# Optimization experiments

Hardware: AMD Instinct MI355X
Metric: run time of the kernel (lower is better)

Reference implementation:

```python
import jax, jax.numpy as jnp
import numpy as np

D_X, D_H, N_I = 1024, 64, 16  # model dim, per-head dim (d_q=d_k=d_v), heads
BSZ, SEQ = 2, 2048


def _linear(x, W, b):
    return x @ W.T + b


def setup_inputs() -> dict:
    key = jax.random.key(0)
    ks = jax.random.split(key, 16)
    s_in = 1.0 / np.sqrt(D_X)
    s_hd = 1.0 / np.sqrt(N_I * D_H)
    return {
        "query": jax.random.normal(ks[0], (BSZ, SEQ, D_X), jnp.float32),
        "key": jax.random.normal(ks[1], (BSZ, SEQ, D_X), jnp.float32),
        "value": jax.random.normal(ks[2], (BSZ, SEQ, D_X), jnp.float32),
        "Wq": jax.random.normal(ks[3], (N_I * D_H, D_X), jnp.float32) * s_in,
        "bq": jnp.zeros((N_I * D_H,), jnp.float32),
        "Wk": jax.random.normal(ks[4], (N_I * D_H, D_X), jnp.float32) * s_in,
        "bk": jnp.zeros((N_I * D_H,), jnp.float32),
        "Wv": jax.random.normal(ks[5], (N_I * D_H, D_X), jnp.float32) * s_in,
        "bv": jnp.zeros((N_I * D_H,), jnp.float32),
        "Wxv": jax.random.normal(ks[6], (N_I * D_H, D_X), jnp.float32) * s_in,
        "bxv": jnp.zeros((N_I * D_H,), jnp.float32),
        "Wxo": jax.random.normal(ks[7], (D_X, N_I * D_H), jnp.float32) * s_hd,
        "bxo": jnp.zeros((D_X,), jnp.float32),
        "Wmo": jax.random.normal(ks[8], (D_X, N_I * D_H), jnp.float32) * s_hd,
        "bmo": jnp.zeros((D_X,), jnp.float32),
    }


def reference(query, key, value, Wq, bq, Wk, bk, Wv, bv, Wxv, bxv, Wxo, bxo, Wmo, bmo):
    bsz, seq, _ = query.shape

    def heads(x):  # (b, s, n_I*d) -> (b, h, s, d)
        return x.reshape(bsz, seq, N_I, D_H).transpose(0, 2, 1, 3)

    Q = heads(_linear(query, Wq, bq))
    K = heads(_linear(key, Wk, bk))
    V = heads(_linear(value, Wv, bv))

    dot = jnp.einsum('bhid,bhjd->bhij', Q, K) / jnp.sqrt(jnp.float32(D_H))
    attention = jax.nn.softmax(dot, axis=-1)  # dropout p=0 (eval)

    # use_xv=True: replace K with xV = W_xv(key) for the k_bar aggregation
    xV = heads(_linear(key, Wxv, bxv))

    k_bar = jnp.einsum('bhjd,bhij->bhid', xV, attention)
    v_bar = jnp.einsum('bhjd,bhij->bhid', V, attention)

    def merge(x):  # (b, h, s, d) -> (b, s, h*d)
        return x.transpose(0, 2, 1, 3).reshape(bsz, seq, N_I * D_H)

    x = _linear(merge(k_bar), Wxo, bxo)
    m = _linear(merge(v_bar), Wmo, bmo)
    return (x, m)
```

## Files before the change

### kernel.cpp

```cpp
#include <hip/hip_runtime.h>
#include <math.h>

typedef __bf16 bf16;
typedef __bf16 bf16x2 __attribute__((ext_vector_type(2)));
typedef __bf16 bf16x4 __attribute__((ext_vector_type(4)));
typedef __bf16 bf16x8 __attribute__((ext_vector_type(8)));
typedef float f32x4 __attribute__((ext_vector_type(4)));

#define SEQ 2048
#define DH 64
#define DX 1024
#define NH 16
#define LP 72

static __device__ __forceinline__ f32x4 mfma16(bf16x8 a, bf16x8 b, f32x4 c) {
    return __builtin_amdgcn_mfma_f32_16x16x32_bf16(a, b, c, 0, 0, 0);
}
static __device__ __forceinline__ bf16x8 cvt8(const float* __restrict__ p) {
    f32x4 a = *(const f32x4*)p;
    f32x4 b = *(const f32x4*)(p + 4);
    bf16x8 r;
    #pragma unroll
    for (int j = 0; j < 4; ++j) { r[j] = (bf16)a[j]; r[4 + j] = (bf16)b[j]; }
    return r;
}

#define GL16(gp, lp) __builtin_amdgcn_global_load_lds( \
    (const __attribute__((address_space(1))) void*)(gp), \
    (__attribute__((address_space(3))) void*)(lp), 16, 0, 0)


__global__ __launch_bounds__(256) void cvt_all(
    const float* __restrict__ q, const float* __restrict__ k,
    const float* __restrict__ v,
    const float* __restrict__ w0, const float* __restrict__ w1,
    const float* __restrict__ w2, const float* __restrict__ w3,
    const float* __restrict__ w4, const float* __restrict__ w5,
    bf16* __restrict__ out)
{
    const size_t i = (size_t)blockIdx.x * 2048 + threadIdx.x * 8;
    const int seg = (int)(i >> 20);
    const float* s;
    size_t off;
    if (seg < 4)       { s = q; off = i; }
    else if (seg < 8)  { s = k; off = i - (4ull << 20); }
    else if (seg < 12) { s = v; off = i - (8ull << 20); }
    else {
        const float* ww[6] = {w0, w1, w2, w3, w4, w5};
        s = ww[seg - 12]; off = i - ((size_t)seg << 20);
    }
    *(bf16x8*)(out + i) = cvt8(s + off);
}

struct G4 {
    const bf16* X[4]; const bf16* W[4]; const float* B[4];
    bf16* Yb[4]; float* Yf[4]; int xmode[4]; int ymode[4];
};

template<int BM>
__global__ __launch_bounds__(512) void gemm256(G4 a)
{
    constexpr int MREP = BM / 32;
    __shared__ __align__(16) bf16 As[2][BM * 64];
    __shared__ __align__(16) bf16 Bs[2][256 * 64];

    const int z = blockIdx.z;
    const bf16* __restrict__ X = a.X[z];
    const bf16* __restrict__ W = a.W[z];
    const int xmode = a.xmode[z], ymode = a.ymode[z];

    const int tid  = threadIdx.x;
    const int wid  = tid >> 6;
    const int lane = tid & 63;
    const int l16  = lane & 15;
    const int quad = lane >> 4;
    const int wm   = wid >> 2;
    const int wn   = wid & 3;

    const int nx = gridDim.x;
    const int nt = nx * gridDim.y;
    int t = blockIdx.x + nx * blockIdx.y;
    t = (t & 7) * (nt >> 3) + (t >> 3);
    const int n0 = (t % nx) * 256;
    const int m0 = (t / nx) * BM;

    const int srow8 = lane >> 3;
    const int sch   = (lane & 7) ^ srow8;

    f32x4 acc[MREP][4];
    #pragma unroll
    for (int i = 0; i < MREP; ++i)
        #pragma unroll
        for (int j = 0; j < 4; ++j) acc[i][j] = (f32x4){0.f,0.f,0.f,0.f};

    auto stage = [&](int buf, int kb) {
        #pragma unroll
        for (int g = 0; g < BM / 64; ++g) {
            const int row = g * 64 + wid * 8 + srow8;
            const bf16* src;
            if (xmode == 0) {
                src = X + (size_t)(m0 + row) * DX + kb * 64 + sch * 8;
            } else {
                const int m = m0 + row;
                const int b = m >> 11, s = m & 2047;
                src = X + ((size_t)(b * NH + kb) * SEQ + s) * DH + sch * 8;
            }
            GL16(src, &As[buf][(g * 64 + wid * 8) * 64]);
        }
        #pragma unroll
        for (int g = 0; g < 4; ++g) {
            const int row = g * 64 + wid * 8 + srow8;
            const bf16* src = W + (size_t)(n0 + row) * DX + kb * 64 + sch * 8;
            GL16(src, &Bs[buf][(g * 64 + wid * 8) * 64]);
        }
    };

    stage(0, 0);
    __syncthreads();

    int cur = 0;
    for (int kb = 0; kb < DX / 64; ++kb) {
        if (kb + 1 < DX / 64) stage(cur ^ 1, kb + 1);
        #pragma unroll
        for (int ks = 0; ks < 2; ++ks) {
            bf16x8 af[MREP], bfr[4];
            const int cc = (ks * 4 + quad) ^ (l16 & 7);
            #pragma unroll
            for (int mf = 0; mf < MREP; ++mf)
                af[mf] = *(const bf16x8*)&As[cur][(wm * (BM/2) + mf * 16 + l16) * 64 + cc * 8];
            #pragma unroll
            for (int nf = 0; nf < 4; ++nf)
                bfr[nf] = *(const bf16x8*)&Bs[cur][(wn * 64 + nf * 16 + l16) * 64 + cc * 8];
            #pragma unroll
            for (int mf = 0; mf < MREP; ++mf)
                #pragma unroll
                for (int nf = 0; nf < 4; ++nf)
                    acc[mf][nf] = mfma16(af[mf], bfr[nf], acc[mf][nf]);
        }
        __syncthreads();
        cur ^= 1;
    }

    #pragma unroll
    for (int nf = 0; nf < 4; ++nf) {
        const int col = n0 + wn * 64 + nf * 16 + l16;
        const float bvv = a.B[z][col];
        #pragma unroll
        for (int mf = 0; mf < MREP; ++mf) {
            #pragma unroll
            for (int r = 0; r < 4; ++r) {
                const int row = m0 + wm * (BM/2) + mf * 16 + quad * 4 + r;
                const float vv = acc[mf][nf][r] + bvv;
                if (ymode == 0) {
                    const int b = row >> 11, s = row & 2047;
                    const int h = col >> 6, d = col & 63;
                    a.Yb[z][((size_t)(b * NH + h) * SEQ + s) * DH + d] = (bf16)vv;
                } else {
                    a.Yf[z][(size_t)row * DX + col] = vv;
                }
            }
        }
    }
}

__global__ __launch_bounds__(512) void attn_pair(
    bf16* __restrict__ Q, const bf16* __restrict__ K,
    const bf16* __restrict__ V, const bf16* __restrict__ xV,
    bf16* __restrict__ VB)
{
    __shared__ __align__(16) bf16 Ks[2][64 * 64];
    __shared__ __align__(16) bf16 Vt [64 * LP];
    __shared__ __align__(16) bf16 xVt[64 * LP];
    __shared__ __align__(16) bf16 Pl[4][32 * LP];

    const int tid  = threadIdx.x;
    const int wid  = tid >> 6;
    const int lane = tid & 63;
    const int l16  = lane & 15;
    const int quad = lane >> 4;
    const int pair = wid >> 1;
    const int half = wid & 1;
    const size_t hb = ((size_t)blockIdx.z * NH + blockIdx.y) * SEQ * DH;
    const int qp = blockIdx.x * 128 + pair * 32;
    const int q0 = qp + half * 16;

    bf16x8 qf[2];
    #pragma unroll
    for (int ks = 0; ks < 2; ++ks)
        qf[ks] = *(const bf16x8*)(Q + hb + (size_t)(q0 + l16) * DH + ks*32 + quad*8);

    bf16x8 one8;
    #pragma unroll
    for (int j = 0; j < 8; ++j) one8[j] = (bf16)1.0f;

    f32x4 ov[2][4];
    f32x4 rsa[2];
    #pragma unroll
    for (int mf = 0; mf < 2; ++mf) {
        rsa[mf] = (f32x4){0.f,0.f,0.f,0.f};
        #pragma unroll
        for (int c = 0; c < 4; ++c) ov[mf][c] = (f32x4){0.f,0.f,0.f,0.f};
    }

    const int krow = lane >> 3;
    const int kch  = (lane & 7) ^ krow;
    const bf16* __restrict__ vsrc = (tid & 256) ? xV : V;
    bf16* __restrict__ vdst = (tid & 256) ? xVt : Vt;
    const int t8  = tid & 255;
    const int vkp = (t8 & 31) * 2;
    const int vd0 = (t8 >> 5) * 8;
    const float SCL = 0.125f * 1.4426950408889634f;

    bf16x8 pv0, pv1;
    {
        const bf16* kg = K + hb + (size_t)(wid*8 + krow) * DH + kch*8;
        GL16(kg, &Ks[0][(wid*8) * 64]);
        const size_t g0 = hb + (size_t)vkp * DH + vd0;
        pv0 = *(const bf16x8*)(vsrc + g0);
        pv1 = *(const bf16x8*)(vsrc + g0 + DH);
    }

    int c = 0;
    for (int kt = 0; kt < SEQ; kt += 64) {
        #pragma unroll
        for (int j = 0; j < 8; ++j)
            *(bf16x2*)&vdst[(vd0 + j) * LP + vkp] = (bf16x2){pv0[j], pv1[j]};
        if (kt + 64 < SEQ) {
            const bf16* kg = K + hb + (size_t)(kt + 64 + wid*8 + krow) * DH + kch*8;
            GL16(kg, &Ks[c ^ 1][(wid*8) * 64]);
            const size_t g0 = hb + (size_t)(kt + 64 + vkp) * DH + vd0;
            pv0 = *(const bf16x8*)(vsrc + g0);
            pv1 = *(const bf16x8*)(vsrc + g0 + DH);
        }
        __asm__ volatile("s_waitcnt lgkmcnt(0)" ::: "memory");
        __builtin_amdgcn_s_barrier();
        __asm__ volatile("s_waitcnt vmcnt(3)" ::: "memory");
        __builtin_amdgcn_sched_barrier(0);

        f32x4 sf[4];
        #pragma unroll
        for (int mf = 0; mf < 4; ++mf) sf[mf] = (f32x4){0.f,0.f,0.f,0.f};
        __builtin_amdgcn_s_setprio(1);
        #pragma unroll
        for (int ks = 0; ks < 2; ++ks)
            #pragma unroll
            for (int mf = 0; mf < 4; ++mf) {
                bf16x8 kf = *(const bf16x8*)&Ks[c][(mf*16 + l16) * 64 +
                                                   (((ks*4 + quad) ^ (l16 & 7)) * 8)];
                sf[mf] = mfma16(kf, qf[ks], sf[mf]);
            }
        __builtin_amdgcn_s_setprio(0);

        #pragma unroll
        for (int mf = 0; mf < 4; ++mf) {
            float p0 = __builtin_amdgcn_exp2f(sf[mf][0] * SCL);
            float p1 = __builtin_amdgcn_exp2f(sf[mf][1] * SCL);
            float p2 = __builtin_amdgcn_exp2f(sf[mf][2] * SCL);
            float p3 = __builtin_amdgcn_exp2f(sf[mf][3] * SCL);
            *(bf16x4*)&Pl[pair][(half*16 + l16) * LP + mf*16 + quad*4] =
                (bf16x4){(bf16)p0, (bf16)p1, (bf16)p2, (bf16)p3};
        }
        __asm__ volatile("s_waitcnt lgkmcnt(0)" ::: "memory");
        __builtin_amdgcn_s_barrier();
        __builtin_amdgcn_sched_barrier(0);

        __builtin_amdgcn_s_setprio(1);
        #pragma unroll
        for (int ks = 0; ks < 2; ++ks) {
            bf16x8 pa[2];
            #pragma unroll
            for (int mf = 0; mf < 2; ++mf)
                pa[mf] = *(const bf16x8*)&Pl[pair][(mf*16 + l16) * LP + ks*32 + quad*8];
            #pragma unroll
            for (int mf = 0; mf < 2; ++mf)
                rsa[mf] = mfma16(pa[mf], one8, rsa[mf]);
            const bf16* __restrict__ tile = half ? xVt : Vt;
            #pragma unroll
            for (int cc = 0; cc < 4; ++cc) {
                bf16x8 bv = *(const bf16x8*)&tile[(cc*16 + l16) * LP + ks*32 + quad*8];
                #pragma unroll
                for (int mf = 0; mf < 2; ++mf)
                    ov[mf][cc] = mfma16(pa[mf], bv, ov[mf][cc]);
            }
        }
        __builtin_amdgcn_s_setprio(0);

        __builtin_amdgcn_sched_barrier(0);
        __builtin_amdgcn_s_barrier();
        c ^= 1;
    }

    bf16* __restrict__ outp = half ? Q : VB;
    #pragma unroll
    for (int mf = 0; mf < 2; ++mf)
        #pragma unroll
        for (int r = 0; r < 4; ++r) {
            const int qrow = mf * 16 + quad * 4 + r;
            const float inv = 1.0f / rsa[mf][r];
            const size_t base = hb + (size_t)(qp + qrow) * DH;
            #pragma unroll
            for (int cc = 0; cc < 4; ++cc)
                outp[base + cc*16 + l16] = (bf16)(ov[mf][cc][r] * inv);
        }
}


__global__ __launch_bounds__(256) void proj_gemm(
    const void* __restrict__ Xv, const float* __restrict__ W,
    const float* __restrict__ bias, void* __restrict__ Yv,
    int in_kind, int out_mode)
{
    __shared__ __align__(16) bf16 As[64 * LP];
    __shared__ __align__(16) bf16 Bs[128 * LP];
    const int tid  = threadIdx.x;
    const int wave = tid >> 6;
    const int lane = tid & 63;
    const int l16  = lane & 15;
    const int quad = lane >> 4;
    const int m0 = blockIdx.y * 64;
    const int n0 = blockIdx.x * 128;
    const int m_w = (wave >> 1) * 32;
    const int n_w = (wave & 1) * 64;
    const int ar = tid >> 2, ac = (tid & 3) * 16;
    const int br = tid >> 1, bc = (tid & 1) * 32;

    f32x4 acc[2][4];
    #pragma unroll
    for (int i = 0; i < 2; ++i)
        #pragma unroll
        for (int j = 0; j < 4; ++j) acc[i][j] = (f32x4){0.f,0.f,0.f,0.f};

    for (int kb = 0; kb < DX / 64; ++kb) {
        __syncthreads();
        if (in_kind == 0) {
            const float* xp = (const float*)Xv + (size_t)(m0 + ar) * DX + kb * 64 + ac;
            *(bf16x8*)&As[ar * LP + ac]     = cvt8(xp);
            *(bf16x8*)&As[ar * LP + ac + 8] = cvt8(xp + 8);
        } else {
            const bf16* xp = (const bf16*)Xv + ((size_t)kb * SEQ + (m0 + ar)) * DH + ac;
            *(bf16x8*)&As[ar * LP + ac]     = *(const bf16x8*)xp;
            *(bf16x8*)&As[ar * LP + ac + 8] = *(const bf16x8*)(xp + 8);
        }
        {
            const float* wp = W + (size_t)(n0 + br) * DX + kb * 64 + bc;
            #pragma unroll
            for (int g = 0; g < 4; ++g)
                *(bf16x8*)&Bs[br * LP + bc + g * 8] = cvt8(wp + g * 8);
        }
        __syncthreads();
        #pragma unroll
        for (int ks = 0; ks < 2; ++ks) {
            bf16x8 a0 = *(const bf16x8*)&As[(m_w + l16)      * LP + ks * 32 + quad * 8];
            bf16x8 a1 = *(const bf16x8*)&As[(m_w + 16 + l16) * LP + ks * 32 + quad * 8];
            #pragma unroll
            for (int nf = 0; nf < 4; ++nf) {
                bf16x8 b = *(const bf16x8*)&Bs[(n_w + nf * 16 + l16) * LP + ks * 32 + quad * 8];
                acc[0][nf] = mfma16(a0, b, acc[0][nf]);
                acc[1][nf] = mfma16(a1, b, acc[1][nf]);
            }
        }
    }
    #pragma unroll
    for (int mf = 0; mf < 2; ++mf)
        #pragma unroll
        for (int nf = 0; nf < 4; ++nf) {
            const int col = n0 + n_w + nf * 16 + l16;
            const float bvv = bias[col];
            #pragma unroll
            for (int r = 0; r < 4; ++r) {
                const int row = m0 + m_w + mf * 16 + quad * 4 + r;
                float v = acc[mf][nf][r] + bvv;
                if (out_mode == 0) {
                    int h = col >> 6, d = col & 63;
                    ((bf16*)Yv)[((size_t)h * SEQ + row) * DH + d] = (bf16)v;
                } else {
                    ((float*)Yv)[(size_t)row * DX + col] = v;
                }
            }
        }
}

__global__ __launch_bounds__(256) void attn_dual(
    bf16* __restrict__ Q, const bf16* __restrict__ K,
    const bf16* __restrict__ V, const bf16* __restrict__ xV,
    bf16* __restrict__ vb)
{
    __shared__ __align__(16) bf16 Ks [64 * LP];
    __shared__ __align__(16) bf16 Vt [64 * LP];
    __shared__ __align__(16) bf16 xVt[64 * LP];
    __shared__ __align__(16) bf16 Pl[4][32 * LP];
    const int tid  = threadIdx.x;
    const int h    = blockIdx.y;
    const int qt   = blockIdx.x;
    const int wave = tid >> 6;
    const int lane = tid & 63;
    const int l16  = lane & 15;
    const int quad = lane >> 4;
    const size_t hb = (size_t)h * SEQ * DH;
    const int q0 = qt * 128 + wave * 32;

    bf16x8 qf[2][2];
    #pragma unroll
    for (int mf = 0; mf < 2; ++mf)
        #pragma unroll
        for (int ks = 0; ks < 2; ++ks)
            qf[mf][ks] = *(const bf16x8*)(Q + hb + (size_t)(q0 + mf*16 + l16) * DH + ks*32 + quad*8);

    float mr[2][4], lr[2][4];
    f32x4 ov[2][4], oxv[2][4];
    #pragma unroll
    for (int mf = 0; mf < 2; ++mf)
        #pragma unroll
        for (int r = 0; r < 4; ++r) { mr[mf][r] = -1e30f; lr[mf][r] = 0.f; }
    #pragma unroll
    for (int mf = 0; mf < 2; ++mf)
        #pragma unroll
        for (int c = 0; c < 4; ++c) {
            ov[mf][c]  = (f32x4){0.f,0.f,0.f,0.f};
            oxv[mf][c] = (f32x4){0.f,0.f,0.f,0.f};
        }
    const int sr = tid >> 2, sc = (tid & 3) * 16;
    const int vkp = (tid & 31) * 2;
    const int vd0 = (tid >> 5) * 8;
    const float SCL = 0.125f * 1.4426950408889634f;

    for (int kt = 0; kt < SEQ; kt += 64) {
        __syncthreads();
        {
            const bf16* kpt = K + hb + (size_t)(kt + sr) * DH + sc;
            *(bf16x8*)&Ks[sr * LP + sc]     = *(const bf16x8*)kpt;
            *(bf16x8*)&Ks[sr * LP + sc + 8] = *(const bf16x8*)(kpt + 8);
            const size_t g0 = hb + (size_t)(kt + vkp) * DH + vd0;
            bf16x8 v0 = *(const bf16x8*)(V + g0);
            bf16x8 v1 = *(const bf16x8*)(V + g0 + DH);
            bf16x8 x0 = *(const bf16x8*)(xV + g0);
            bf16x8 x1 = *(const bf16x8*)(xV + g0 + DH);
            #pragma unroll
            for (int j = 0; j < 8; ++j) {
                *(bf16x2*)&Vt [(vd0 + j) * LP + vkp] = (bf16x2){v0[j], v1[j]};
                *(bf16x2*)&xVt[(vd0 + j) * LP + vkp] = (bf16x2){x0[j], x1[j]};
            }
        }
        __syncthreads();
        f32x4 sf[2][4];
        #pragma unroll
        for (int mf = 0; mf < 2; ++mf)
            #pragma unroll
            for (int nf = 0; nf < 4; ++nf) sf[mf][nf] = (f32x4){0.f,0.f,0.f,0.f};
        #pragma unroll
        for (int ks = 0; ks < 2; ++ks)
            #pragma unroll
            for (int nf = 0; nf < 4; ++nf) {
                bf16x8 bk = *(const bf16x8*)&Ks[(nf * 16 + l16) * LP + ks * 32 + quad * 8];
                sf[0][nf] = mfma16(qf[0][ks], bk, sf[0][nf]);
                sf[1][nf] = mfma16(qf[1][ks], bk, sf[1][nf]);
            }
        float mx[2][4], rs[2][4], alpha[2][4];
        #pragma unroll
        for (int mf = 0; mf < 2; ++mf)
            #pragma unroll
            for (int r = 0; r < 4; ++r) {
                float aa = fmaxf(sf[mf][0][r], sf[mf][1][r]);
                float bb = fmaxf(sf[mf][2][r], sf[mf][3][r]);
                mx[mf][r] = fmaxf(aa, bb) * SCL;
            }
        #pragma unroll
        for (int off = 1; off < 16; off <<= 1)
            #pragma unroll
            for (int mf = 0; mf < 2; ++mf)
                #pragma unroll
                for (int r = 0; r < 4; ++r)
                    mx[mf][r] = fmaxf(mx[mf][r], __shfl_xor(mx[mf][r], off, 64));
        #pragma unroll
        for (int mf = 0; mf < 2; ++mf)
            #pragma unroll
            for (int r = 0; r < 4; ++r) {
                float mnew = fmaxf(mr[mf][r], mx[mf][r]);
                alpha[mf][r] = exp2f(mr[mf][r] - mnew);
                mr[mf][r] = mnew;
            }
        bf16* pw = &Pl[wave][0];
        #pragma unroll
        for (int mf = 0; mf < 2; ++mf)
            #pragma unroll
            for (int r = 0; r < 4; ++r) rs[mf][r] = 0.f;
        #pragma unroll
        for (int mf = 0; mf < 2; ++mf)
            #pragma unroll
            for (int nf = 0; nf < 4; ++nf)
                #pragma unroll
                for (int r = 0; r < 4; ++r) {
                    float p = exp2f(sf[mf][nf][r] * SCL - mr[mf][r]);
                    rs[mf][r] += p;
                    pw[(mf * 16 + quad * 4 + r) * LP + nf * 16 + l16] = (bf16)p;
                }
        #pragma unroll
        for (int off = 1; off < 16; off <<= 1)
            #pragma unroll
            for (int mf = 0; mf < 2; ++mf)
                #pragma unroll
                for (int r = 0; r < 4; ++r)
                    rs[mf][r] += __shfl_xor(rs[mf][r], off, 64);
        #pragma unroll
        for (int mf = 0; mf < 2; ++mf)
            #pragma unroll
            for (int r = 0; r < 4; ++r)
                lr[mf][r] = lr[mf][r] * alpha[mf][r] + rs[mf][r];
        #pragma unroll
        for (int mf = 0; mf < 2; ++mf)
            #pragma unroll
            for (int c = 0; c < 4; ++c)
                #pragma unroll
                for (int r = 0; r < 4; ++r) {
                    ov[mf][c][r]  *= alpha[mf][r];
                    oxv[mf][c][r] *= alpha[mf][r];
                }
        __asm__ volatile("s_waitcnt lgkmcnt(0)" ::: "memory");
        #pragma unroll
        for (int ks = 0; ks < 2; ++ks) {
            bf16x8 pa0 = *(const bf16x8*)&Pl[wave][(l16)      * LP + ks * 32 + quad * 8];
            bf16x8 pa1 = *(const bf16x8*)&Pl[wave][(16 + l16) * LP + ks * 32 + quad * 8];
            #pragma unroll
            for (int c = 0; c < 4; ++c) {
                bf16x8 bv = *(const bf16x8*)&Vt [(c * 16 + l16) * LP + ks * 32 + quad * 8];
                ov[0][c]  = mfma16(pa0, bv, ov[0][c]);
                ov[1][c]  = mfma16(pa1, bv, ov[1][c]);
                bf16x8 bx = *(const bf16x8*)&xVt[(c * 16 + l16) * LP + ks * 32 + quad * 8];
                oxv[0][c] = mfma16(pa0, bx, oxv[0][c]);
                oxv[1][c] = mfma16(pa1, bx, oxv[1][c]);
            }
        }
    }
    #pragma unroll
    for (int mf = 0; mf < 2; ++mf)
        #pragma unroll
        for (int r = 0; r < 4; ++r) {
            const int s = q0 + mf * 16 + quad * 4 + r;
            const float inv = 1.0f / lr[mf][r];
            #pragma unroll
            for (int c = 0; c < 4; ++c) {
                const int d = c * 16 + l16;
                Q [hb + (size_t)s * DH + d] = (bf16)(oxv[mf][c][r] * inv);
                vb[hb + (size_t)s * DH + d] = (bf16)(ov[mf][c][r]  * inv);
            }
        }
}


extern "C" void kernel_launch(void* const* d_in, const int* in_sizes, int n_in,
                              void* d_out, int out_size, void* d_ws, size_t ws_size,
                              hipStream_t stream) {
    const float* query = (const float*)d_in[0];
    const float* key   = (const float*)d_in[1];
    const float* value = (const float*)d_in[2];
    const float* Wq  = (const float*)d_in[3];  const float* bq  = (const float*)d_in[4];
    const float* Wk  = (const float*)d_in[5];  const float* bk  = (const float*)d_in[6];
    const float* Wv  = (const float*)d_in[7];  const float* bv  = (const float*)d_in[8];
    const float* Wxv = (const float*)d_in[9];  const float* bxv = (const float*)d_in[10];
    const float* Wxo = (const float*)d_in[11]; const float* bxo = (const float*)d_in[12];
    const float* Wmo = (const float*)d_in[13]; const float* bmo = (const float*)d_in[14];

    float* out = (float*)d_out;
    const size_t SB = (size_t)SEQ * DX;
    const size_t M1 = 1ull << 20;

    dim3 blk(256);

    if (ws_size >= (76ull << 20)) {
        bf16* ws = (bf16*)d_ws;
        bf16* qb  = ws;
        bf16* kb  = ws + 4 * M1;
        bf16* vb  = ws + 8 * M1;
        bf16* Wqb = ws + 12 * M1;
        bf16* Wkb = Wqb + M1;
        bf16* Wvb = Wkb + M1;
        bf16* Wxvb= Wvb + M1;
        bf16* Wxob= Wxvb + M1;
        bf16* Wmob= Wxob + M1;
        bf16* Qs  = ws + 18 * M1;
        bf16* Kss = ws + 22 * M1;
        bf16* Vs  = ws + 26 * M1;
        bf16* xVs = ws + 30 * M1;
        bf16* VBs = ws + 34 * M1;

        cvt_all<<<9216, blk, 0, stream>>>(query, key, value,
                                          Wq, Wk, Wv, Wxv, Wxo, Wmo, ws + 0);

        G4 g1;
        g1.X[0]=qb;  g1.W[0]=Wqb;  g1.B[0]=bq;  g1.Yb[0]=Qs;  g1.Yf[0]=nullptr; g1.xmode[0]=0; g1.ymode[0]=0;
        g1.X[1]=kb;  g1.W[1]=Wkb;  g1.B[1]=bk;  g1.Yb[1]=Kss; g1.Yf[1]=nullptr; g1.xmode[1]=0; g1.ymode[1]=0;
        g1.X[2]=vb;  g1.W[2]=Wvb;  g1.B[2]=bv;  g1.Yb[2]=Vs;  g1.Yf[2]=nullptr; g1.xmode[2]=0; g1.ymode[2]=0;
        g1.X[3]=kb;  g1.W[3]=Wxvb; g1.B[3]=bxv; g1.Yb[3]=xVs; g1.Yf[3]=nullptr; g1.xmode[3]=0; g1.ymode[3]=0;
        gemm256<256><<<dim3(4, 16, 4), dim3(512), 0, stream>>>(g1);

        attn_pair<<<dim3(16, NH, 2), dim3(512), 0, stream>>>(Qs, Kss, Vs, xVs, VBs);

        G4 g2;
        g2.X[0]=Qs;  g2.W[0]=Wxob; g2.B[0]=bxo; g2.Yb[0]=nullptr; g2.Yf[0]=out;          g2.xmode[0]=1; g2.ymode[0]=1;
        g2.X[1]=VBs; g2.W[1]=Wmob; g2.B[1]=bmo; g2.Yb[1]=nullptr; g2.Yf[1]=out + 2*SB;   g2.xmode[1]=1; g2.ymode[1]=1;
        g2.X[2]=Qs;  g2.W[2]=Wxob; g2.B[2]=bxo; g2.Yb[2]=nullptr; g2.Yf[2]=out;          g2.xmode[2]=1; g2.ymode[2]=1;
        g2.X[3]=Qs;  g2.W[3]=Wxob; g2.B[3]=bxo; g2.Yb[3]=nullptr; g2.Yf[3]=out;          g2.xmode[3]=1; g2.ymode[3]=1;
        gemm256<128><<<dim3(4, 32, 2), dim3(512), 0, stream>>>(g2);
    } else {
        bf16* Qs  = (bf16*)d_ws;
        bf16* Ksb = Qs  + SB;
        bf16* Vs  = Ksb + SB;
        bf16* xVs = Vs  + SB;
        bf16* vbs = xVs + SB;
        dim3 pg(8, 32);
        dim3 ag(16, NH);
        for (int b = 0; b < 2; ++b) {
            const float* q_b = query + (size_t)b * SB;
            const float* k_b = key   + (size_t)b * SB;
            const float* v_b = value + (size_t)b * SB;
            float* x_b = out + (size_t)b * SB;
            float* m_b = out + 2 * SB + (size_t)b * SB;
            proj_gemm<<<pg, blk, 0, stream>>>(q_b, Wq,  bq,  Qs,  0, 0);
            proj_gemm<<<pg, blk, 0, stream>>>(k_b, Wk,  bk,  Ksb, 0, 0);
            proj_gemm<<<pg, blk, 0, stream>>>(v_b, Wv,  bv,  Vs,  0, 0);
            proj_gemm<<<pg, blk, 0, stream>>>(k_b, Wxv, bxv, xVs, 0, 0);
            attn_dual<<<ag, blk, 0, stream>>>(Qs, Ksb, Vs, xVs, vbs);
            proj_gemm<<<pg, blk, 0, stream>>>(Qs,  Wxo, bxo, x_b, 1, 1);
            proj_gemm<<<pg, blk, 0, stream>>>(vbs, Wmo, bmo, m_b, 1, 1);
        }
    }
}
```

Baseline: 283.6 us.

## Pipeline GEMM loads with vmcnt waits and stage bf16 epilogue through LDS

The GEMM main loop now waits only on the previous stage's global-to-LDS loads with a partial vmcnt instead of a full __syncthreads, so the next tile's loads stay in flight during compute. The bf16 head-layout epilogue now writes through a padded LDS buffer and stores 16-byte vectors, replacing scattered 2-byte stores. The attention kernel's vmcnt wait moves before the barrier for correctness of the async loads. The change risks miscounted vmcnt values and adds LDS round-trips in the epilogue.

Result: faster. 265.5 us (-6.4%).

```diff
diff --git a/kernel.cpp b/kernel.cpp
--- a/kernel.cpp
+++ b/kernel.cpp
@@ -61,8 +61,11 @@
 __global__ __launch_bounds__(512) void gemm256(G4 a)
 {
     constexpr int MREP = BM / 32;
-    __shared__ __align__(16) bf16 As[2][BM * 64];
-    __shared__ __align__(16) bf16 Bs[2][256 * 64];
+    constexpr int NT   = DX / 64;
+    constexpr int AEL  = BM * 64;
+    constexpr int BEL  = 256 * 64;
+    constexpr int SN   = BM / 64 + 4;
+    __shared__ __align__(16) bf16 smem[2 * AEL + 2 * BEL];
 
     const int z = blockIdx.z;
     const bf16* __restrict__ X = a.X[z];
@@ -94,6 +97,8 @@
         for (int j = 0; j < 4; ++j) acc[i][j] = (f32x4){0.f,0.f,0.f,0.f};
 
     auto stage = [&](int buf, int kb) {
+        bf16* Ab = smem + buf * AEL;
+        bf16* Bb = smem + 2 * AEL + buf * BEL;
         #pragma unroll
         for (int g = 0; g < BM / 64; ++g) {
             const int row = g * 64 + wid * 8 + srow8;
@@ -105,58 +110,104 @@
                 const int b = m >> 11, s = m & 2047;
                 src = X + ((size_t)(b * NH + kb) * SEQ + s) * DH + sch * 8;
             }
-            GL16(src, &As[buf][(g * 64 + wid * 8) * 64]);
+            GL16(src, Ab + (g * 64 + wid * 8) * 64);
         }
         #pragma unroll
         for (int g = 0; g < 4; ++g) {
             const int row = g * 64 + wid * 8 + srow8;
             const bf16* src = W + (size_t)(n0 + row) * DX + kb * 64 + sch * 8;
-            GL16(src, &Bs[buf][(g * 64 + wid * 8) * 64]);
+            GL16(src, Bb + (g * 64 + wid * 8) * 64);
         }
     };
 
     stage(0, 0);
-    __syncthreads();
 
     int cur = 0;
-    for (int kb = 0; kb < DX / 64; ++kb) {
-        if (kb + 1 < DX / 64) stage(cur ^ 1, kb + 1);
+    for (int kb = 0; kb < NT; ++kb) {
+        if (kb + 1 < NT) {
+            stage(cur ^ 1, kb + 1);
+            if constexpr (SN == 8) {
+                __asm__ volatile("s_waitcnt vmcnt(8)" ::: "memory");
+            } else {
+                __asm__ volatile("s_waitcnt vmcnt(6)" ::: "memory");
+            }
+        } else {
+            __asm__ volatile("s_waitcnt vmcnt(0)" ::: "memory");
+        }
+        __builtin_amdgcn_s_barrier();
+        __builtin_amdgcn_sched_barrier(0);
+
+        const bf16* Ab = smem + cur * AEL;
+        const bf16* Bb = smem + 2 * AEL + cur * BEL;
         #pragma unroll
         for (int ks = 0; ks < 2; ++ks) {
             bf16x8 af[MREP], bfr[4];
             const int cc = (ks * 4 + quad) ^ (l16 & 7);
             #pragma unroll
             for (int mf = 0; mf < MREP; ++mf)
-                af[mf] = *(const bf16x8*)&As[cur][(wm * (BM/2) + mf * 16 + l16) * 64 + cc * 8];
+                af[mf] = *(const bf16x8*)&Ab[(wm * (BM/2) + mf * 16 + l16) * 64 + cc * 8];
             #pragma unroll
             for (int nf = 0; nf < 4; ++nf)
-                bfr[nf] = *(const bf16x8*)&Bs[cur][(wn * 64 + nf * 16 + l16) * 64 + cc * 8];
+                bfr[nf] = *(const bf16x8*)&Bb[(wn * 64 + nf * 16 + l16) * 64 + cc * 8];
             #pragma unroll
             for (int mf = 0; mf < MREP; ++mf)
                 #pragma unroll
                 for (int nf = 0; nf < 4; ++nf)
                     acc[mf][nf] = mfma16(af[mf], bfr[nf], acc[mf][nf]);
         }
-        __syncthreads();
+        __builtin_amdgcn_sched_barrier(0);
+        __builtin_amdgcn_s_barrier();
         cur ^= 1;
     }
 
-    #pragma unroll
-    for (int nf = 0; nf < 4; ++nf) {
-        const int col = n0 + wn * 64 + nf * 16 + l16;
-        const float bvv = a.B[z][col];
-        #pragma unroll
-        for (int mf = 0; mf < MREP; ++mf) {
-            #pragma unroll
-            for (int r = 0; r < 4; ++r) {
-                const int row = m0 + wm * (BM/2) + mf * 16 + quad * 4 + r;
-                const float vv = acc[mf][nf][r] + bvv;
-                if (ymode == 0) {
-                    const int b = row >> 11, s = row & 2047;
-                    const int h = col >> 6, d = col & 63;
-                    a.Yb[z][((size_t)(b * NH + h) * SEQ + s) * DH + d] = (bf16)vv;
-                } else {
-                    a.Yf[z][(size_t)row * DX + col] = vv;
+    if (ymode == 0) {
+        constexpr int EPS = 264;
+        constexpr int PR  = 128;
+        constexpr int NP  = BM / PR;
+        bf16* Ep = smem;
+        #pragma unroll
+        for (int p = 0; p < NP; ++p) {
+            __builtin_amdgcn_s_barrier();
+            if (NP == 1 || wm == p) {
+                #pragma unroll
+                for (int nf = 0; nf < 4; ++nf) {
+                    const int col = wn * 64 + nf * 16 + l16;
+                    const float bvv = a.B[z][n0 + col];
+                    #pragma unroll
+                    for (int mf = 0; mf < MREP; ++mf) {
+                        const int rb = wm * (BM/2) + mf * 16 + quad * 4 - p * PR;
+                        #pragma unroll
+                        for (int r = 0; r < 4; ++r)
+                            Ep[(rb + r) * EPS + col] = (bf16)(acc[mf][nf][r] + bvv);
+                    }
+                }
+            }
+            __asm__ volatile("s_waitcnt lgkmcnt(0)" ::: "memory");
+            __builtin_amdgcn_s_barrier();
+            #pragma unroll
+            for (int j = 0; j < 8; ++j) {
+                const int g    = j * 512 + tid;
+                const int lrow = g >> 5;
+                const int cg   = g & 31;
+                bf16x8 vv = *(const bf16x8*)&Ep[lrow * EPS + cg * 8];
+                const int row = m0 + p * PR + lrow;
+                const int b = row >> 11, s = row & 2047;
+                const int col = n0 + cg * 8;
+                const int h = col >> 6, d = col & 63;
+                *(bf16x8*)&a.Yb[z][((size_t)(b * NH + h) * SEQ + s) * DH + d] = vv;
+            }
+        }
+    } else {
+        #pragma unroll
+        for (int nf = 0; nf < 4; ++nf) {
+            const int col = n0 + wn * 64 + nf * 16 + l16;
+            const float bvv = a.B[z][col];
+            #pragma unroll
+            for (int mf = 0; mf < MREP; ++mf) {
+                #pragma unroll
+                for (int r = 0; r < 4; ++r) {
+                    const int row = m0 + wm * (BM/2) + mf * 16 + quad * 4 + r;
+                    a.Yf[z][(size_t)row * DX + col] = acc[mf][nf][r] + bvv;
                 }
             }
         }
@@ -233,8 +284,8 @@
             pv1 = *(const bf16x8*)(vsrc + g0 + DH);
         }
         __asm__ volatile("s_waitcnt lgkmcnt(0)" ::: "memory");
+        __asm__ volatile("s_waitcnt vmcnt(3)" ::: "memory");
         __builtin_amdgcn_s_barrier();
-        __asm__ volatile("s_waitcnt vmcnt(3)" ::: "memory");
         __builtin_amdgcn_sched_barrier(0);
 
         f32x4 sf[4];
```
